# Performance work log

Hardware: AMD Instinct MI355X
Metric: run time of the kernel (lower is better)

The kernel has to match this reference:

```python
import jax, jax.numpy as jnp
import numpy as np

B, N, MODES, WIDTH = 4, 8192, 12, 32
TWO = 2 * MODES  # 24
M_TOT = TWO * (TWO - 1)  # 552


def setup_inputs() -> dict:
    key = jax.random.key(0)
    ks = jax.random.split(key, 12)
    scale = 1.0 / (WIDTH * WIDTH)
    x = jax.random.uniform(ks[0], (B, N, 2), jnp.float32)
    fc0_w = jax.random.normal(ks[1], (2, WIDTH), jnp.float32) * 0.1
    fc0_b = jax.random.normal(ks[2], (WIDTH,), jnp.float32) * 0.05
    # 4 layers x {weights1, weights2}, stored as real/imag pairs (torch.rand cfloat ~ U[0,1)+1j*U[0,1))
    spec_w = jax.random.uniform(ks[3], (4, 2, WIDTH, WIDTH, MODES, MODES, 2), jnp.float32) * scale
    conv_w = jax.random.normal(ks[4], (4, WIDTH, WIDTH), jnp.float32) * 0.1  # Conv1d k=1 -> [O,I]
    conv_b = jax.random.normal(ks[5], (4, WIDTH), jnp.float32) * 0.05
    fc1_w = jax.random.normal(ks[6], (WIDTH, 128), jnp.float32) * 0.1
    fc1_b = jax.random.normal(ks[7], (128,), jnp.float32) * 0.05
    fc2_w = jax.random.normal(ks[8], (128, 1), jnp.float32) * 0.1
    fc2_b = jax.random.normal(ks[9], (1,), jnp.float32) * 0.05
    return {"x": x, "fc0_w": fc0_w, "fc0_b": fc0_b, "spec_w": spec_w,
            "conv_w": conv_w, "conv_b": conv_b, "fc1_w": fc1_w, "fc1_b": fc1_b,
            "fc2_w": fc2_w, "fc2_b": fc2_b}


def _vft_matrices(xp, yp):
    # xp, yp: [B, N], already min-shifted and scaled to [0, 6.28]
    kx = jnp.concatenate([jnp.arange(MODES), jnp.arange(-MODES, 0)]).astype(jnp.float32)       # [24]
    ky = jnp.concatenate([jnp.arange(MODES), jnp.arange(-(MODES - 1), 0)]).astype(jnp.float32)  # [23]
    Xm = kx[None, :, None] * xp[:, None, :]  # [B,24,N]
    Ym = ky[None, :, None] * yp[:, None, :]  # [B,23,N]
    # torch: X repeat(1,23,1) tiles blocks; Y repeat(1,1,24).reshape interleaves -> row j*24+i = X[i]+Y[j]
    phase = jnp.tile(Xm, (1, TWO - 1, 1)) + jnp.repeat(Ym, TWO, axis=1)  # [B,552,N]
    V_fwd = jnp.exp(-1j * phase)                    # [B,552,N] complex64
    V_inv = jnp.conj(V_fwd).transpose(0, 2, 1)      # [B,N,552]
    return V_fwd, V_inv


def _spectral_conv(h, V_fwd, V_inv, w1, w2):
    # h: [B,C,N] real; w1,w2: [C,C,M,M] complex
    b, c, n = h.shape
    # forward Vandermonde transform: bmm(V_fwd, h^T) then permute -> [B,C,552]
    x_ft = jnp.einsum('bmn,bnc->bcm', V_fwd, h.astype(jnp.complex64).transpose(0, 2, 1))
    x_ft = x_ft.reshape(b, c, TWO, TWO - 1)
    top = jnp.einsum('bixy,ioxy->boxy', x_ft[:, :, :MODES, :MODES], w1)
    bot = jnp.einsum('bixy,ioxy->boxy', x_ft[:, :, -MODES:, :MODES], w2)
    out_ft = jnp.zeros((b, WIDTH, TWO, MODES), jnp.complex64)
    out_ft = out_ft.at[:, :, :MODES, :MODES].set(top)
    out_ft = out_ft.at[:, :, -MODES:, :MODES].set(bot)
    x_ft = out_ft.reshape(b, WIDTH, 2 * MODES * MODES)  # [B,C,288]
    # conjugate-symmetric completion (flip over last two dims, as in source)
    x_ft2 = jnp.conj(jnp.flip(x_ft[..., TWO:], axis=(-2, -1)))  # [B,C,264]
    x_ft = jnp.concatenate([x_ft, x_ft2], axis=-1)  # [B,C,552]
    out = jnp.einsum('bnm,bmc->bcn', V_inv, x_ft.transpose(0, 2, 1))  # [B,C,N]
    return (out / n * 2).real


def reference(x, fc0_w, fc0_b, spec_w, conv_w, conv_b, fc1_w, fc1_b, fc2_w, fc2_b):
    gelu = lambda t: jax.nn.gelu(t, approximate=False)
    # VFT mutates x in-place by subtracting global mins (view semantics in torch)
    xp = x[:, :, 0] - jnp.min(x[:, :, 0])
    yp = x[:, :, 1] - jnp.min(x[:, :, 1])
    x_in = jnp.stack([xp, yp], axis=-1)  # what fc0 actually sees
    V_fwd, V_inv = _vft_matrices(xp * 6.28 / jnp.max(xp), yp * 6.28 / jnp.max(yp))
    h = (x_in @ fc0_w + fc0_b).transpose(0, 2, 1)  # [B,C,N]
    for l in range(4):
        w1 = spec_w[l, 0, ..., 0] + 1j * spec_w[l, 0, ..., 1]
        w2 = spec_w[l, 1, ..., 0] + 1j * spec_w[l, 1, ..., 1]
        x1 = _spectral_conv(h, V_fwd, V_inv, w1, w2)
        x2 = jnp.einsum('bin,oi->bon', h, conv_w[l]) + conv_b[l][None, :, None]
        h = x1 + x2
        if l < 3:
            h = gelu(h)
    h = h.transpose(0, 2, 1)  # [B,N,C]
    h = gelu(h @ fc1_w + fc1_b)
    return h @ fc2_w + fc2_b  # [B,N,1]
```

## Files before the change

### kernel.cpp

```cpp
#include <hip/hip_runtime.h>
#include <cmath>

#define NB 4
#define NN 8192
#define CH 32

typedef short short8 __attribute__((ext_vector_type(8)));
typedef float floatx4 __attribute__((ext_vector_type(4)));
typedef unsigned short ushort_t;

__device__ __forceinline__ unsigned short f2b(float f){
  unsigned u = __float_as_uint(f);
  u = u + 0x7FFFu + ((u >> 16) & 1u);
  return (unsigned short)(u >> 16);
}
__device__ __forceinline__ float b2f(unsigned short h){
  return __uint_as_float(((unsigned)h) << 16);
}
__device__ __forceinline__ float gelu_f(float v){
  return 0.5f * v * (1.0f + erff(v * 0.70710678118654752440f));
}
__device__ __forceinline__ int repk(int t){
  int j = t / 24, i = t - j * 24;
  if(j == 0)  return (i <= 12) ? i : -1;
  if(j <= 11) return 13 + (j - 1) * 24 + i;
  return (i == 12) ? 277 + (j - 12) : -1;
}
__device__ __forceinline__ int partner(int t){
  int j = t / 24, i = t - j * 24;
  return ((23 - j) % 23) * 24 + ((24 - i) % 24);
}
__device__ __forceinline__ int repT(int k){
  if(k < 13) return k;
  if(k < 277){ int m = k - 13; return (m / 24 + 1) * 24 + (m % 24); }
  return (k - 277 + 12) * 24 + 12;
}

__global__ __launch_bounds__(256) void k_pre(const float* __restrict__ spec,
    float2* __restrict__ wt, const float* __restrict__ x, float4* __restrict__ pmm)
{
  const int tid = threadIdx.x;
  if(blockIdx.x < 128){
    int g = blockIdx.x * 256 + tid;
    float a = x[(size_t)g * 2], b = x[(size_t)g * 2 + 1];
    float mn0 = a, mx0 = a, mn1 = b, mx1 = b;
    for(int off = 32; off > 0; off >>= 1){
      mn0 = fminf(mn0, __shfl_down(mn0, off));
      mx0 = fmaxf(mx0, __shfl_down(mx0, off));
      mn1 = fminf(mn1, __shfl_down(mn1, off));
      mx1 = fmaxf(mx1, __shfl_down(mx1, off));
    }
    __shared__ float4 wp[4];
    if((tid & 63) == 0) wp[tid >> 6] = make_float4(mn0, mn1, mx0, mx1);
    __syncthreads();
    if(tid == 0){
      float4 r = wp[0];
      for(int i2 = 1; i2 < 4; ++i2){
        float4 v = wp[i2];
        r.x = fminf(r.x, v.x); r.y = fminf(r.y, v.y);
        r.z = fmaxf(r.z, v.z); r.w = fmaxf(r.w, v.w);
      }
      pmm[blockIdx.x] = r;
    }
  } else {
    int g = (blockIdx.x - 128) * 256 + tid;
    int o  = g & 31;
    int i  = (g >> 5) & 31;
    int rest = g >> 10;
    int pq = rest % 144;
    int ls = rest / 144;
    wt[g] = ((const float2*)spec)[(((size_t)(ls * 32 + i) * 32 + o) * 144 + pq)];
  }
}

__global__ __launch_bounds__(256) void k_vbuild(const float* __restrict__ x,
    const float4* __restrict__ pmm, const float* __restrict__ fw,
    const float* __restrict__ fb, ushort_t* __restrict__ AF, ushort_t* __restrict__ VTF,
    float* __restrict__ h, ushort_t* __restrict__ hb)
{
  __shared__ ushort_t lds1[32 * 584];
  __shared__ float4 mmv;
  const int tid = threadIdx.x;
  if(tid < 64){
    float4 a = pmm[tid], c = pmm[tid + 64];
    float mn0 = fminf(a.x, c.x), mn1 = fminf(a.y, c.y);
    float mx0 = fmaxf(a.z, c.z), mx1 = fmaxf(a.w, c.w);
    for(int off = 32; off > 0; off >>= 1){
      mn0 = fminf(mn0, __shfl_down(mn0, off));
      mn1 = fminf(mn1, __shfl_down(mn1, off));
      mx0 = fmaxf(mx0, __shfl_down(mx0, off));
      mx1 = fmaxf(mx1, __shfl_down(mx1, off));
    }
    if(tid == 0) mmv = make_float4(mn0, mn1, mx0, mx1);
  }
  __syncthreads();
  const int nl = tid & 31, part = tid >> 5;
  const int b = blockIdx.x >> 8;
  const int nblk = blockIdx.x & 255;
  const int n = nblk * 32 + nl;
  float mn0 = mmv.x, mn1 = mmv.y, mx0 = mmv.z, mx1 = mmv.w;
  float x0 = x[(size_t)(b * NN + n) * 2]     - mn0;
  float x1 = x[(size_t)(b * NN + n) * 2 + 1] - mn1;
  float sp = x0 * (6.28f / (mx0 - mn0));
  float sq = x1 * (6.28f / (mx1 - mn1));
  float cx, sx, cy, sy;
  sincosf(sp, &sx, &cx);
  sincosf(sq, &sy, &cy);
  int j0 = part * 3;
  int j1 = (j0 + 3 < 23) ? j0 + 3 : 23;
  float ky0 = (j0 < 12) ? (float)j0 : (float)(j0 - 23);
  float cb, sb;
  sincosf(ky0 * sq, &sb, &cb);
  for(int j = j0; j < j1; ++j){
    float ca = 1.0f, sa = 0.0f;
    #pragma unroll
    for(int i = 0; i < 24; ++i){
      float vr = ca * cb - sa * sb;
      float vi = -(sa * cb + ca * sb);
      int t = j * 24 + i;
      int k = repk(t);
      if(k >= 0){
        lds1[nl * 584 + k]       = f2b(vr);
        lds1[nl * 584 + 288 + k] = f2b(vi);
      }
      float cn = ca * cx - sa * sx;
      float sn = sa * cx + ca * sx;
      if(i == 11) sn = -sn;
      ca = cn; sa = sn;
    }
    float cbn = cb * cy - sb * sy;
    float sbn = sb * cy + cb * sy;
    cb = cbn; sb = sbn;
  }
  __syncthreads();
  #pragma unroll
  for(int r = 0; r < 9; ++r){
    int c = tid + 256 * r;
    int t16 = c / 1152;
    int c2 = c - t16 * 1152;
    int kk = c2 >> 6;
    int rem = c2 & 63;
    int q = rem >> 4, n15 = rem & 15;
    short8 v = *(const short8*)(lds1 + (t16 * 16 + n15) * 584 + kk * 32 + q * 8);
    *(short8*)(VTF + ((size_t)((b * 512 + nblk * 2 + t16) * 18 + kk)) * 512
               + (q * 16 + n15) * 8) = v;
  }
  #pragma unroll
  for(int r = 0; r < 9; ++r){
    int c = tid + 256 * r;
    int st = c >> 6;
    int rem = c & 63;
    int q = rem >> 4, srow = rem & 15;
    int sg = st * 16 + srow;
    int s = (sg < 288) ? sg : sg - 288;
    int sinh_ = (sg >= 288);
    int p2 = s / 12, qq = s - p2 * 12;
    int t = p2 * 23 + qq;
    int k = repk(t);
    unsigned short flip = 0;
    if(k < 0){ k = repk(partner(t)); if(sinh_) flip = 0x8000; }
    int col = sinh_ ? 288 + k : k;
    ushort_t tmp[8];
    #pragma unroll
    for(int e = 0; e < 8; ++e)
      tmp[e] = lds1[(q * 8 + e) * 584 + col] ^ flip;
    *(short8*)(AF + ((size_t)((b * 36 + st) * 256 + nblk)) * 512
               + (q * 16 + srow) * 8) = *(short8*)tmp;
  }
  #pragma unroll
  for(int rr = 0; rr < 4; ++rr){
    int c2 = (tid >> 5) + rr * 8;
    float v = fb[c2] + x0 * fw[c2] + x1 * fw[32 + c2];
    size_t idx = (size_t)(b * CH + c2) * NN + n;
    h[idx] = v; hb[idx] = f2b(v);
  }
}

__global__ __launch_bounds__(256) void k_fwd(const ushort_t* __restrict__ AF,
    const ushort_t* __restrict__ hb, float* __restrict__ xp)
{
  const int stp = blockIdx.x;
  const int ks = blockIdx.y;
  const int b  = blockIdx.z;
  const int w = threadIdx.x >> 6;
  const int lane = threadIdx.x & 63;
  const int row = lane & 15;
  const int q = lane >> 4;
  const int st0 = stp * 2;
  const size_t abase0 = ((size_t)(b * 36 + st0) * 256) * 512 + (q * 16 + row) * 8;
  const size_t abase1 = abase0 + (size_t)256 * 512;
  const size_t hb0 = (size_t)(b * CH + row) * NN;
  const size_t hb1 = hb0 + (size_t)16 * NN;
  floatx4 aA0 = {0.f,0.f,0.f,0.f}, aA1 = {0.f,0.f,0.f,0.f};
  floatx4 aB0 = {0.f,0.f,0.f,0.f}, aB1 = {0.f,0.f,0.f,0.f};
  #pragma unroll
  for(int kk = 0; kk < 8; ++kk){
    int g = ks * 32 + w * 8 + kk;
    short8 A0 = *(const short8*)(AF + abase0 + (size_t)g * 512);
    short8 A1 = *(const short8*)(AF + abase1 + (size_t)g * 512);
    int nn2 = g * 32 + q * 8;
    short8 B0 = *(const short8*)(hb + hb0 + nn2);
    short8 B1 = *(const short8*)(hb + hb1 + nn2);
    aA0 = __builtin_amdgcn_mfma_f32_16x16x32_bf16(A0, B0, aA0, 0, 0, 0);
    aA1 = __builtin_amdgcn_mfma_f32_16x16x32_bf16(A0, B1, aA1, 0, 0, 0);
    aB0 = __builtin_amdgcn_mfma_f32_16x16x32_bf16(A1, B0, aB0, 0, 0, 0);
    aB1 = __builtin_amdgcn_mfma_f32_16x16x32_bf16(A1, B1, aB1, 0, 0, 0);
  }
  __shared__ float red[4 * 512];
  const int e = threadIdx.x;
  #pragma unroll
  for(int r = 0; r < 4; ++r){
    int rrow = q * 4 + r;
    red[w * 512 + rrow * 32 + row]      = aA0[r];
    red[w * 512 + rrow * 32 + 16 + row] = aA1[r];
  }
  __syncthreads();
  {
    float v0 = red[e] + red[512 + e] + red[1024 + e] + red[1536 + e];
    float v1 = red[e + 256] + red[512 + e + 256] + red[1024 + e + 256] + red[1536 + e + 256];
    size_t base = ((size_t)(ks * NB + b) * 576 + st0 * 16) * 32;
    xp[base + e] = v0;
    xp[base + e + 256] = v1;
  }
  __syncthreads();
  #pragma unroll
  for(int r = 0; r < 4; ++r){
    int rrow = q * 4 + r;
    red[w * 512 + rrow * 32 + row]      = aB0[r];
    red[w * 512 + rrow * 32 + 16 + row] = aB1[r];
  }
  __syncthreads();
  {
    float v0 = red[e] + red[512 + e] + red[1024 + e] + red[1536 + e];
    float v1 = red[e + 256] + red[512 + e + 256] + red[1024 + e + 256] + red[1536 + e + 256];
    size_t base = ((size_t)(ks * NB + b) * 576 + (st0 + 1) * 16) * 32;
    xp[base + e] = v0;
    xp[base + e + 256] = v1;
  }
}

__global__ __launch_bounds__(256) void k_mixg(const float* __restrict__ xp,
    const float2* __restrict__ wt, ushort_t* __restrict__ ghi, ushort_t* __restrict__ glo,
    int layer)
{
  const int w = threadIdx.x >> 6;
  const int lane = threadIdx.x & 63;
  const int k = blockIdx.x * 4 + w;
  const int b = blockIdx.y;
  const int t = repT(k);
  const int j = t / 24, i = t - j * 24;
  const int u = partner(t);
  const bool unpaired = (i == 12) || (u == t);
  const int idxT = (t < 288) ? t : 575 - t;  const bool cfT = (t >= 288);
  const int idxU = (u < 288) ? u : 575 - u;  const bool cfU = (u >= 288);
  __shared__ float Xs[4][2][64];
  const int o = lane & 31, half = lane >> 5;
  #pragma unroll
  for(int m = 0; m < 2; ++m){
    int idx = m ? idxU : idxT;
    int rrow = half ? 288 + idx : idx;
    float s = 0.f;
    #pragma unroll
    for(int ks = 0; ks < 8; ++ks)
      s += xp[((size_t)(ks * NB + b) * 576 + rrow) * 32 + o];
    Xs[w][m][half * 32 + o] = s;
  }
  __syncthreads();
  float Fr[2], Fi[2];
  #pragma unroll
  for(int m = 0; m < 2; ++m){
    int idx = m ? idxU : idxT;
    int p2 = idx / 12, qq = idx - p2 * 12;
    int sel = (p2 < 12) ? 0 : 1;
    int pq = (p2 % 12) * 12 + qq;
    const float2* wb = wt + ((size_t)((layer * 2 + sel) * 144 + pq)) * 1024;
    int i0 = half * 16;
    float fr = 0.f, fi = 0.f;
    #pragma unroll
    for(int ii = 0; ii < 16; ++ii){
      int i2 = i0 + ii;
      float xr = Xs[w][m][i2], xi = Xs[w][m][32 + i2];
      float2 wv = wb[i2 * 32 + o];
      fr += xr * wv.x - xi * wv.y;
      fi += xr * wv.y + xi * wv.x;
    }
    fr += __shfl_down(fr, 32);
    fi += __shfl_down(fi, 32);
    Fr[m] = fr; Fi[m] = fi;
  }
  const int c = lane & 31;
  const int srcT = cfT ? 31 - c : c;
  const int srcU = cfU ? 31 - c : c;
  float fax = __shfl(Fr[0], srcT);
  float fay = __shfl(Fi[0], srcT);
  float fbx = __shfl(Fr[1], srcU);
  float fby = __shfl(Fi[1], srcU);
  if(lane < 32){
    float gr = fax;
    float gi = cfT ? -fay : fay;
    if(!unpaired){
      gr += fbx;
      gi -= (cfU ? -fby : fby);
    }
    unsigned short hr = f2b(gr); float lr = gr - b2f(hr);
    unsigned short hi2 = f2b(gi); float li = gi - b2f(hi2);
    size_t base = (size_t)(b * CH + c) * 576;
    ghi[base + k] = hr;          ghi[base + 288 + k] = hi2;
    glo[base + k] = f2b(lr);     glo[base + 288 + k] = f2b(li);
  }
}

template<int LAST>
__global__ __launch_bounds__(512, 2) void k_inv(const ushort_t* __restrict__ VTF,
    const ushort_t* __restrict__ ghi, const ushort_t* __restrict__ glo,
    const float* __restrict__ hfull, const float* __restrict__ cw,
    const float* __restrict__ cbias, float* __restrict__ hout,
    ushort_t* __restrict__ houtb, int layer,
    const float* __restrict__ w1, const float* __restrict__ b1,
    const float* __restrict__ w2, const float* __restrict__ b2,
    float* __restrict__ out)
{
  __shared__ ushort_t GH[32][584];
  __shared__ ushort_t GL[32][584];
  __shared__ float hTc[32][129];
  __shared__ float Wl[1024];
  __shared__ float Bl[32];
  const int tid = threadIdx.x;
  const int b = blockIdx.y;
  const int n0 = blockIdx.x * 128;
  for(int idx = tid; idx < 2304; idx += 512){
    int ch = idx / 72, g8 = (idx - ch * 72) * 8;
    size_t src = (size_t)(b * CH + ch) * 576 + g8;
    *(short8*)&GH[ch][g8] = *(const short8*)(ghi + src);
    *(short8*)&GL[ch][g8] = *(const short8*)(glo + src);
  }
  {
    int ch = tid >> 4, grp = tid & 15;
    const float* src = hfull + (size_t)(b * CH + ch) * NN + n0 + grp * 8;
    float4 v0 = *(const float4*)src;
    float4 v1 = *(const float4*)(src + 4);
    int p = grp * 8;
    hTc[ch][p + 0] = v0.x; hTc[ch][p + 1] = v0.y;
    hTc[ch][p + 2] = v0.z; hTc[ch][p + 3] = v0.w;
    hTc[ch][p + 4] = v1.x; hTc[ch][p + 5] = v1.y;
    hTc[ch][p + 6] = v1.z; hTc[ch][p + 7] = v1.w;
  }
  for(int idx = tid; idx < 1024; idx += 512)
    Wl[(idx & 31) * 32 + (idx >> 5)] = cw[layer * 1024 + idx];
  if(tid < 32) Bl[tid] = cbias[layer * 32 + tid];
  __syncthreads();
  const int lane = tid & 63;
  const int w = tid >> 6;
  const int row = lane & 15;
  const int q = lane >> 4;
  const int nloc = w * 16 + row;
  const int n = n0 + nloc;
  const int n16 = blockIdx.x * 8 + w;
  const ushort_t* vb = VTF + ((size_t)(b * 512 + n16) * 18) * 512 + (q * 16 + row) * 8;
  const int ko = q * 8;
  floatx4 acc0 = {0.f,0.f,0.f,0.f}, acc1 = {0.f,0.f,0.f,0.f};
  #pragma unroll
  for(int kk = 0; kk < 18; ++kk){
    short8 Bv  = *(const short8*)(vb + (size_t)kk * 512);
    short8 Ah0 = *(const short8*)&GH[row][ko + kk * 32];
    short8 Al0 = *(const short8*)&GL[row][ko + kk * 32];
    short8 Ah1 = *(const short8*)&GH[16 + row][ko + kk * 32];
    short8 Al1 = *(const short8*)&GL[16 + row][ko + kk * 32];
    acc0 = __builtin_amdgcn_mfma_f32_16x16x32_bf16(Ah0, Bv, acc0, 0, 0, 0);
    acc0 = __builtin_amdgcn_mfma_f32_16x16x32_bf16(Al0, Bv, acc0, 0, 0, 0);
    acc1 = __builtin_amdgcn_mfma_f32_16x16x32_bf16(Ah1, Bv, acc1, 0, 0, 0);
    acc1 = __builtin_amdgcn_mfma_f32_16x16x32_bf16(Al1, Bv, acc1, 0, 0, 0);
  }
  float acc2[8];
  {
    const int c0 = q * 4;
    #pragma unroll
    for(int r = 0; r < 4; ++r){ acc2[r] = Bl[c0 + r]; acc2[4 + r] = Bl[16 + c0 + r]; }
    #pragma unroll
    for(int i = 0; i < CH; ++i){
      float hv = hTc[i][nloc];
      float4 wv0 = *(const float4*)&Wl[i * 32 + c0];
      float4 wv1 = *(const float4*)&Wl[i * 32 + 16 + c0];
      acc2[0] = fmaf(hv, wv0.x, acc2[0]);
      acc2[1] = fmaf(hv, wv0.y, acc2[1]);
      acc2[2] = fmaf(hv, wv0.z, acc2[2]);
      acc2[3] = fmaf(hv, wv0.w, acc2[3]);
      acc2[4] = fmaf(hv, wv1.x, acc2[4]);
      acc2[5] = fmaf(hv, wv1.y, acc2[5]);
      acc2[6] = fmaf(hv, wv1.z, acc2[6]);
      acc2[7] = fmaf(hv, wv1.w, acc2[7]);
    }
  }
  const float sc = 2.0f / 8192.0f;
  if constexpr(!LAST){
    #pragma unroll
    for(int r = 0; r < 4; ++r){
      int c = q * 4 + r;
      float v0 = gelu_f(acc0[r] * sc + acc2[r]);
      size_t idx0 = (size_t)(b * CH + c) * NN + n;
      hout[idx0] = v0; houtb[idx0] = f2b(v0);
      float v1 = gelu_f(acc1[r] * sc + acc2[4 + r]);
      size_t idx1 = (size_t)(b * CH + 16 + c) * NN + n;
      hout[idx1] = v1; houtb[idx1] = f2b(v1);
    }
  } else {
    __shared__ float hT2[128][33];
    __shared__ float Wfc1[4096];
    __shared__ float b1s[128], w2s[128];
    __shared__ float red2[512];
    #pragma unroll
    for(int r = 0; r < 4; ++r){
      int c = q * 4 + r;
      hT2[nloc][c]      = acc0[r] * sc + acc2[r];
      hT2[nloc][16 + c] = acc1[r] * sc + acc2[4 + r];
    }
    for(int idx2 = tid; idx2 < 4096; idx2 += 512) Wfc1[idx2] = w1[idx2];
    if(tid < 128){ b1s[tid] = b1[tid]; w2s[tid] = w2[tid]; }
    __syncthreads();
    const int nl2 = tid & 127;
    const int js = tid >> 7;
    float acc3 = 0.f;
    for(int jj = js * 32; jj < js * 32 + 32; ++jj){
      float s = b1s[jj];
      #pragma unroll
      for(int i = 0; i < CH; ++i) s = fmaf(hT2[nl2][i], Wfc1[i * 128 + jj], s);
      acc3 = fmaf(gelu_f(s), w2s[jj], acc3);
    }
    red2[tid] = acc3;
    __syncthreads();
    if(js == 0){
      float v = red2[nl2] + red2[nl2 + 128] + red2[nl2 + 256] + red2[nl2 + 384] + b2[0];
      out[(size_t)b * NN + n0 + nl2] = v;
    }
  }
}

extern "C" void kernel_launch(void* const* d_in, const int* in_sizes, int n_in,
                              void* d_out, int out_size, void* d_ws, size_t ws_size,
                              hipStream_t stream)
{
  const float* x      = (const float*)d_in[0];
  const float* fc0_w  = (const float*)d_in[1];
  const float* fc0_b  = (const float*)d_in[2];
  const float* spec_w = (const float*)d_in[3];
  const float* conv_w = (const float*)d_in[4];
  const float* conv_b = (const float*)d_in[5];
  const float* fc1_w  = (const float*)d_in[6];
  const float* fc1_b  = (const float*)d_in[7];
  const float* fc2_w  = (const float*)d_in[8];
  const float* fc2_b  = (const float*)d_in[9];
  float* out = (float*)d_out;

  char* w = (char*)d_ws;
  const size_t OFF_PMM  = 0;
  const size_t OFF_WT   = 4096;
  const size_t OFF_AF   = OFF_WT  + 9437184;
  const size_t OFF_VTF  = OFF_AF  + 37748736;
  const size_t OFF_H0   = OFF_VTF + 37748736;
  const size_t OFF_H1   = OFF_H0  + 4194304;
  const size_t OFF_H0B  = OFF_H1  + 4194304;
  const size_t OFF_H1B  = OFF_H0B + 2097152;
  const size_t OFF_XP   = OFF_H1B + 2097152;
  const size_t OFF_GHI  = OFF_XP  + 2359296;
  const size_t OFF_GLO  = OFF_GHI + 147456;

  float4* pmm    = (float4*)(w + OFF_PMM);
  float2* wt     = (float2*)(w + OFF_WT);
  ushort_t* AF   = (ushort_t*)(w + OFF_AF);
  ushort_t* VTF  = (ushort_t*)(w + OFF_VTF);
  float* hbuf[2]     = { (float*)(w + OFF_H0), (float*)(w + OFF_H1) };
  ushort_t* hbufb[2] = { (ushort_t*)(w + OFF_H0B), (ushort_t*)(w + OFF_H1B) };
  float* xp      = (float*)(w + OFF_XP);
  ushort_t* ghi  = (ushort_t*)(w + OFF_GHI);
  ushort_t* glo  = (ushort_t*)(w + OFF_GLO);

  hipLaunchKernelGGL(k_pre, dim3(4736), dim3(256), 0, stream, spec_w, wt, x, pmm);
  hipLaunchKernelGGL(k_vbuild, dim3(1024), dim3(256), 0, stream, x, pmm,
                     fc0_w, fc0_b, AF, VTF, hbuf[0], hbufb[0]);

  for(int l = 0; l < 4; ++l){
    int in = l & 1, outb = 1 - in;
    hipLaunchKernelGGL(k_fwd, dim3(18, 8, NB), dim3(256), 0, stream, AF, hbufb[in], xp);
    hipLaunchKernelGGL(k_mixg, dim3(72, NB), dim3(256), 0, stream, xp, wt, ghi, glo, l);
    if(l < 3)
      hipLaunchKernelGGL(k_inv<0>, dim3(64, NB), dim3(512), 0, stream, VTF, ghi, glo,
                         hbuf[in], conv_w, conv_b, hbuf[outb], hbufb[outb], l,
                         fc1_w, fc1_b, fc2_w, fc2_b, out);
    else
      hipLaunchKernelGGL(k_inv<1>, dim3(64, NB), dim3(512), 0, stream, VTF, ghi, glo,
                         hbuf[in], conv_w, conv_b, hbuf[outb], hbufb[outb], l,
                         fc1_w, fc1_b, fc2_w, fc2_b, out);
  }
  (void)in_sizes; (void)n_in; (void)out_size; (void)ws_size;
}
```

Before: 256.2 us.

## Fuse all stages into one cooperative persistent kernel with grid syncs

```diff
diff --git a/kernel.cpp b/kernel.cpp
--- a/kernel.cpp
+++ b/kernel.cpp
@@ -1,5 +1,8 @@
 #include <hip/hip_runtime.h>
+#include <hip/hip_cooperative_groups.h>
 #include <cmath>
+
+namespace cg = cooperative_groups;
 
 #define NB 4
 #define NN 8192
@@ -36,34 +39,49 @@
   return (k - 277 + 12) * 24 + 12;
 }
 
-__global__ __launch_bounds__(256) void k_pre(const float* __restrict__ spec,
-    float2* __restrict__ wt, const float* __restrict__ x, float4* __restrict__ pmm)
+#define SMEM_BYTES 95488
+
+__global__ __launch_bounds__(512, 2) void k_mega(
+    const float* __restrict__ x, const float* __restrict__ fc0w,
+    const float* __restrict__ fc0b, const float* __restrict__ spec,
+    const float* __restrict__ convw, const float* __restrict__ convb,
+    const float* __restrict__ w1, const float* __restrict__ b1,
+    const float* __restrict__ w2, const float* __restrict__ b2,
+    float* __restrict__ out,
+    float2* __restrict__ wt, float4* __restrict__ pmm,
+    ushort_t* __restrict__ AF, ushort_t* __restrict__ VTF,
+    float* __restrict__ h0, float* __restrict__ h1,
+    ushort_t* __restrict__ h0b, ushort_t* __restrict__ h1b,
+    float* __restrict__ xp, ushort_t* __restrict__ ghi, ushort_t* __restrict__ glo)
 {
+  __shared__ __align__(16) char smem[SMEM_BYTES];
+  cg::grid_group grid = cg::this_grid();
   const int tid = threadIdx.x;
-  if(blockIdx.x < 128){
-    int g = blockIdx.x * 256 + tid;
-    float a = x[(size_t)g * 2], b = x[(size_t)g * 2 + 1];
-    float mn0 = a, mx0 = a, mn1 = b, mx1 = b;
+
+  if(blockIdx.x < 64){
+    int g = blockIdx.x * 512 + tid;
+    float a = x[(size_t)g * 2], bb = x[(size_t)g * 2 + 1];
+    float mn0 = a, mx0 = a, mn1 = bb, mx1 = bb;
     for(int off = 32; off > 0; off >>= 1){
       mn0 = fminf(mn0, __shfl_down(mn0, off));
       mx0 = fmaxf(mx0, __shfl_down(mx0, off));
       mn1 = fminf(mn1, __shfl_down(mn1, off));
       mx1 = fmaxf(mx1, __shfl_down(mx1, off));
     }
-    __shared__ float4 wp[4];
+    float4* wp = (float4*)smem;
     if((tid & 63) == 0) wp[tid >> 6] = make_float4(mn0, mn1, mx0, mx1);
     __syncthreads();
     if(tid == 0){
       float4 r = wp[0];
-      for(int i2 = 1; i2 < 4; ++i2){
+      for(int i2 = 1; i2 < 8; ++i2){
         float4 v = wp[i2];
         r.x = fminf(r.x, v.x); r.y = fminf(r.y, v.y);
         r.z = fmaxf(r.z, v.z); r.w = fmaxf(r.w, v.w);
       }
       pmm[blockIdx.x] = r;
     }
-  } else {
-    int g = (blockIdx.x - 128) * 256 + tid;
+  }
+  for(int g = blockIdx.x * 512 + tid; g < 1179648; g += 131072){
     int o  = g & 31;
     int i  = (g >> 5) & 31;
     int rest = g >> 10;
@@ -71,367 +89,380 @@
     int ls = rest / 144;
     wt[g] = ((const float2*)spec)[(((size_t)(ls * 32 + i) * 32 + o) * 144 + pq)];
   }
-}
-
-__global__ __launch_bounds__(256) void k_vbuild(const float* __restrict__ x,
-    const float4* __restrict__ pmm, const float* __restrict__ fw,
-    const float* __restrict__ fb, ushort_t* __restrict__ AF, ushort_t* __restrict__ VTF,
-    float* __restrict__ h, ushort_t* __restrict__ hb)
-{
-  __shared__ ushort_t lds1[32 * 584];
-  __shared__ float4 mmv;
-  const int tid = threadIdx.x;
-  if(tid < 64){
-    float4 a = pmm[tid], c = pmm[tid + 64];
-    float mn0 = fminf(a.x, c.x), mn1 = fminf(a.y, c.y);
-    float mx0 = fmaxf(a.z, c.z), mx1 = fmaxf(a.w, c.w);
-    for(int off = 32; off > 0; off >>= 1){
-      mn0 = fminf(mn0, __shfl_down(mn0, off));
-      mn1 = fminf(mn1, __shfl_down(mn1, off));
-      mx0 = fmaxf(mx0, __shfl_down(mx0, off));
-      mx1 = fmaxf(mx1, __shfl_down(mx1, off));
-    }
-    if(tid == 0) mmv = make_float4(mn0, mn1, mx0, mx1);
+  grid.sync();
+
+  {
+    float4* mmvp = (float4*)(smem + 74752);
+    if(tid < 64){
+      float4 a = pmm[tid];
+      float mn0 = a.x, mn1 = a.y, mx0 = a.z, mx1 = a.w;
+      for(int off = 32; off > 0; off >>= 1){
+        mn0 = fminf(mn0, __shfl_down(mn0, off));
+        mn1 = fminf(mn1, __shfl_down(mn1, off));
+        mx0 = fmaxf(mx0, __shfl_down(mx0, off));
+        mx1 = fmaxf(mx1, __shfl_down(mx1, off));
+      }
+      if(tid == 0) *mmvp = make_float4(mn0, mn1, mx0, mx1);
+    }
+    __syncthreads();
+    const float4 mm = *mmvp;
+    ushort_t* lds1 = (ushort_t*)smem;
+    const int nl = tid & 63, part = tid >> 6;
+    for(int it = 0; it < 2; ++it){
+      int sblk = blockIdx.x * 2 + it;
+      int b = sblk >> 7;
+      int sb = sblk & 127;
+      int n0 = sb * 64;
+      int n = n0 + nl;
+      float x0 = x[(size_t)(b * NN + n) * 2]     - mm.x;
+      float x1 = x[(size_t)(b * NN + n) * 2 + 1] - mm.y;
+      float sp = x0 * (6.28f / (mm.z - mm.x));
+      float sq = x1 * (6.28f / (mm.w - mm.y));
+      float cx, sx, cy, sy;
+      sincosf(sp, &sx, &cx);
+      sincosf(sq, &sy, &cy);
+      int j0 = part * 3;
+      int j1 = (j0 + 3 < 23) ? j0 + 3 : 23;
+      float ky0 = (j0 < 12) ? (float)j0 : (float)(j0 - 23);
+      float cb, sb2;
+      sincosf(ky0 * sq, &sb2, &cb);
+      for(int j = j0; j < j1; ++j){
+        float ca = 1.0f, sa = 0.0f;
+        #pragma unroll
+        for(int i = 0; i < 24; ++i){
+          float vr = ca * cb - sa * sb2;
+          float vi = -(sa * cb + ca * sb2);
+          int t = j * 24 + i;
+          int k = repk(t);
+          if(k >= 0){
+            lds1[nl * 584 + k]       = f2b(vr);
+            lds1[nl * 584 + 288 + k] = f2b(vi);
+          }
+          float cn = ca * cx - sa * sx;
+          float sn = sa * cx + ca * sx;
+          if(i == 11) sn = -sn;
+          ca = cn; sa = sn;
+        }
+        float cbn = cb * cy - sb2 * sy;
+        float sbn = sb2 * cy + cb * sy;
+        cb = cbn; sb2 = sbn;
+      }
+      __syncthreads();
+      #pragma unroll
+      for(int r = 0; r < 9; ++r){
+        int c = tid + 512 * r;
+        int t16 = c / 1152;
+        int c2 = c - t16 * 1152;
+        int kk = c2 >> 6;
+        int rem = c2 & 63;
+        int q = rem >> 4, n15 = rem & 15;
+        short8 v = *(const short8*)(lds1 + (t16 * 16 + n15) * 584 + kk * 32 + q * 8);
+        *(short8*)(VTF + ((size_t)((b * 512 + sb * 4 + t16) * 18 + kk)) * 512
+                   + (q * 16 + n15) * 8) = v;
+      }
+      #pragma unroll
+      for(int r = 0; r < 9; ++r){
+        int c = tid + 512 * r;
+        int hh = c / 2304;
+        int c2 = c - hh * 2304;
+        int st = c2 >> 6;
+        int rem = c2 & 63;
+        int q = rem >> 4, srow = rem & 15;
+        int sg = st * 16 + srow;
+        int s = (sg < 288) ? sg : sg - 288;
+        int sinh_ = (sg >= 288);
+        int p2 = s / 12, qq = s - p2 * 12;
+        int t = p2 * 23 + qq;
+        int k = repk(t);
+        unsigned short flip = 0;
+        if(k < 0){ k = repk(partner(t)); if(sinh_) flip = 0x8000; }
+        int col = sinh_ ? 288 + k : k;
+        ushort_t tmp[8];
+        #pragma unroll
+        for(int e = 0; e < 8; ++e)
+          tmp[e] = lds1[(hh * 32 + q * 8 + e) * 584 + col] ^ flip;
+        *(short8*)(AF + ((size_t)((b * 36 + st) * 256 + sb * 2 + hh)) * 512
+                   + (q * 16 + srow) * 8) = *(short8*)tmp;
+      }
+      #pragma unroll
+      for(int rr = 0; rr < 4; ++rr){
+        int c2 = part + rr * 8;
+        float v = fc0b[c2] + x0 * fc0w[c2] + x1 * fc0w[32 + c2];
+        size_t idx = (size_t)(b * CH + c2) * NN + n;
+        h0[idx] = v; h0b[idx] = f2b(v);
+      }
+      __syncthreads();
+    }
   }
-  __syncthreads();
-  const int nl = tid & 31, part = tid >> 5;
-  const int b = blockIdx.x >> 8;
-  const int nblk = blockIdx.x & 255;
-  const int n = nblk * 32 + nl;
-  float mn0 = mmv.x, mn1 = mmv.y, mx0 = mmv.z, mx1 = mmv.w;
-  float x0 = x[(size_t)(b * NN + n) * 2]     - mn0;
-  float x1 = x[(size_t)(b * NN + n) * 2 + 1] - mn1;
-  float sp = x0 * (6.28f / (mx0 - mn0));
-  float sq = x1 * (6.28f / (mx1 - mn1));
-  float cx, sx, cy, sy;
-  sincosf(sp, &sx, &cx);
-  sincosf(sq, &sy, &cy);
-  int j0 = part * 3;
-  int j1 = (j0 + 3 < 23) ? j0 + 3 : 23;
-  float ky0 = (j0 < 12) ? (float)j0 : (float)(j0 - 23);
-  float cb, sb;
-  sincosf(ky0 * sq, &sb, &cb);
-  for(int j = j0; j < j1; ++j){
-    float ca = 1.0f, sa = 0.0f;
-    #pragma unroll
-    for(int i = 0; i < 24; ++i){
-      float vr = ca * cb - sa * sb;
-      float vi = -(sa * cb + ca * sb);
-      int t = j * 24 + i;
-      int k = repk(t);
-      if(k >= 0){
-        lds1[nl * 584 + k]       = f2b(vr);
-        lds1[nl * 584 + 288 + k] = f2b(vi);
-      }
-      float cn = ca * cx - sa * sx;
-      float sn = sa * cx + ca * sx;
-      if(i == 11) sn = -sn;
-      ca = cn; sa = sn;
-    }
-    float cbn = cb * cy - sb * sy;
-    float sbn = sb * cy + cb * sy;
-    cb = cbn; sb = sbn;
-  }
-  __syncthreads();
-  #pragma unroll
-  for(int r = 0; r < 9; ++r){
-    int c = tid + 256 * r;
-    int t16 = c / 1152;
-    int c2 = c - t16 * 1152;
-    int kk = c2 >> 6;
-    int rem = c2 & 63;
-    int q = rem >> 4, n15 = rem & 15;
-    short8 v = *(const short8*)(lds1 + (t16 * 16 + n15) * 584 + kk * 32 + q * 8);
-    *(short8*)(VTF + ((size_t)((b * 512 + nblk * 2 + t16) * 18 + kk)) * 512
-               + (q * 16 + n15) * 8) = v;
-  }
-  #pragma unroll
-  for(int r = 0; r < 9; ++r){
-    int c = tid + 256 * r;
-    int st = c >> 6;
-    int rem = c & 63;
-    int q = rem >> 4, srow = rem & 15;
-    int sg = st * 16 + srow;
-    int s = (sg < 288) ? sg : sg - 288;
-    int sinh_ = (sg >= 288);
-    int p2 = s / 12, qq = s - p2 * 12;
-    int t = p2 * 23 + qq;
-    int k = repk(t);
-    unsigned short flip = 0;
-    if(k < 0){ k = repk(partner(t)); if(sinh_) flip = 0x8000; }
-    int col = sinh_ ? 288 + k : k;
-    ushort_t tmp[8];
-    #pragma unroll
-    for(int e = 0; e < 8; ++e)
-      tmp[e] = lds1[(q * 8 + e) * 584 + col] ^ flip;
-    *(short8*)(AF + ((size_t)((b * 36 + st) * 256 + nblk)) * 512
-               + (q * 16 + srow) * 8) = *(short8*)tmp;
-  }
-  #pragma unroll
-  for(int rr = 0; rr < 4; ++rr){
-    int c2 = (tid >> 5) + rr * 8;
-    float v = fb[c2] + x0 * fw[c2] + x1 * fw[32 + c2];
-    size_t idx = (size_t)(b * CH + c2) * NN + n;
-    h[idx] = v; hb[idx] = f2b(v);
-  }
-}
-
-__global__ __launch_bounds__(256) void k_fwd(const ushort_t* __restrict__ AF,
-    const ushort_t* __restrict__ hb, float* __restrict__ xp)
-{
-  const int stp = blockIdx.x;
-  const int ks = blockIdx.y;
-  const int b  = blockIdx.z;
-  const int w = threadIdx.x >> 6;
-  const int lane = threadIdx.x & 63;
-  const int row = lane & 15;
-  const int q = lane >> 4;
-  const int st0 = stp * 2;
-  const size_t abase0 = ((size_t)(b * 36 + st0) * 256) * 512 + (q * 16 + row) * 8;
-  const size_t abase1 = abase0 + (size_t)256 * 512;
-  const size_t hb0 = (size_t)(b * CH + row) * NN;
-  const size_t hb1 = hb0 + (size_t)16 * NN;
-  floatx4 aA0 = {0.f,0.f,0.f,0.f}, aA1 = {0.f,0.f,0.f,0.f};
-  floatx4 aB0 = {0.f,0.f,0.f,0.f}, aB1 = {0.f,0.f,0.f,0.f};
-  #pragma unroll
-  for(int kk = 0; kk < 8; ++kk){
-    int g = ks * 32 + w * 8 + kk;
-    short8 A0 = *(const short8*)(AF + abase0 + (size_t)g * 512);
-    short8 A1 = *(const short8*)(AF + abase1 + (size_t)g * 512);
-    int nn2 = g * 32 + q * 8;
-    short8 B0 = *(const short8*)(hb + hb0 + nn2);
-    short8 B1 = *(const short8*)(hb + hb1 + nn2);
-    aA0 = __builtin_amdgcn_mfma_f32_16x16x32_bf16(A0, B0, aA0, 0, 0, 0);
-    aA1 = __builtin_amdgcn_mfma_f32_16x16x32_bf16(A0, B1, aA1, 0, 0, 0);
-    aB0 = __builtin_amdgcn_mfma_f32_16x16x32_bf16(A1, B0, aB0, 0, 0, 0);
-    aB1 = __builtin_amdgcn_mfma_f32_16x16x32_bf16(A1, B1, aB1, 0, 0, 0);
-  }
-  __shared__ float red[4 * 512];
-  const int e = threadIdx.x;
-  #pragma unroll
-  for(int r = 0; r < 4; ++r){
-    int rrow = q * 4 + r;
-    red[w * 512 + rrow * 32 + row]      = aA0[r];
-    red[w * 512 + rrow * 32 + 16 + row] = aA1[r];
-  }
-  __syncthreads();
-  {
-    float v0 = red[e] + red[512 + e] + red[1024 + e] + red[1536 + e];
-    float v1 = red[e + 256] + red[512 + e + 256] + red[1024 + e + 256] + red[1536 + e + 256];
-    size_t base = ((size_t)(ks * NB + b) * 576 + st0 * 16) * 32;
-    xp[base + e] = v0;
-    xp[base + e + 256] = v1;
-  }
-  __syncthreads();
-  #pragma unroll
-  for(int r = 0; r < 4; ++r){
-    int rrow = q * 4 + r;
-    red[w * 512 + rrow * 32 + row]      = aB0[r];
-    red[w * 512 + rrow * 32 + 16 + row] = aB1[r];
-  }
-  __syncthreads();
-  {
-    float v0 = red[e] + red[512 + e] + red[1024 + e] + red[1536 + e];
-    float v1 = red[e + 256] + red[512 + e + 256] + red[1024 + e + 256] + red[1536 + e + 256];
-    size_t base = ((size_t)(ks * NB + b) * 576 + (st0 + 1) * 16) * 32;
-    xp[base + e] = v0;
-    xp[base + e + 256] = v1;
-  }
-}
-
-__global__ __launch_bounds__(256) void k_mixg(const float* __restrict__ xp,
-    const float2* __restrict__ wt, ushort_t* __restrict__ ghi, ushort_t* __restrict__ glo,
-    int layer)
-{
-  const int w = threadIdx.x >> 6;
-  const int lane = threadIdx.x & 63;
-  const int k = blockIdx.x * 4 + w;
-  const int b = blockIdx.y;
-  const int t = repT(k);
-  const int j = t / 24, i = t - j * 24;
-  const int u = partner(t);
-  const bool unpaired = (i == 12) || (u == t);
-  const int idxT = (t < 288) ? t : 575 - t;  const bool cfT = (t >= 288);
-  const int idxU = (u < 288) ? u : 575 - u;  const bool cfU = (u >= 288);
-  __shared__ float Xs[4][2][64];
-  const int o = lane & 31, half = lane >> 5;
-  #pragma unroll
-  for(int m = 0; m < 2; ++m){
-    int idx = m ? idxU : idxT;
-    int rrow = half ? 288 + idx : idx;
-    float s = 0.f;
-    #pragma unroll
-    for(int ks = 0; ks < 8; ++ks)
-      s += xp[((size_t)(ks * NB + b) * 576 + rrow) * 32 + o];
-    Xs[w][m][half * 32 + o] = s;
-  }
-  __syncthreads();
-  float Fr[2], Fi[2];
-  #pragma unroll
-  for(int m = 0; m < 2; ++m){
-    int idx = m ? idxU : idxT;
-    int p2 = idx / 12, qq = idx - p2 * 12;
-    int sel = (p2 < 12) ? 0 : 1;
-    int pq = (p2 % 12) * 12 + qq;
-    const float2* wb = wt + ((size_t)((layer * 2 + sel) * 144 + pq)) * 1024;
-    int i0 = half * 16;
-    float fr = 0.f, fi = 0.f;
-    #pragma unroll
-    for(int ii = 0; ii < 16; ++ii){
-      int i2 = i0 + ii;
-      float xr = Xs[w][m][i2], xi = Xs[w][m][32 + i2];
-      float2 wv = wb[i2 * 32 + o];
-      fr += xr * wv.x - xi * wv.y;
-      fi += xr * wv.y + xi * wv.x;
-    }
-    fr += __shfl_down(fr, 32);
-    fi += __shfl_down(fi, 32);
-    Fr[m] = fr; Fi[m] = fi;
-  }
-  const int c = lane & 31;
-  const int srcT = cfT ? 31 - c : c;
-  const int srcU = cfU ? 31 - c : c;
-  float fax = __shfl(Fr[0], srcT);
-  float fay = __shfl(Fi[0], srcT);
-  float fbx = __shfl(Fr[1], srcU);
-  float fby = __shfl(Fi[1], srcU);
-  if(lane < 32){
-    float gr = fax;
-    float gi = cfT ? -fay : fay;
-    if(!unpaired){
-      gr += fbx;
-      gi -= (cfU ? -fby : fby);
-    }
-    unsigned short hr = f2b(gr); float lr = gr - b2f(hr);
-    unsigned short hi2 = f2b(gi); float li = gi - b2f(hi2);
-    size_t base = (size_t)(b * CH + c) * 576;
-    ghi[base + k] = hr;          ghi[base + 288 + k] = hi2;
-    glo[base + k] = f2b(lr);     glo[base + 288 + k] = f2b(li);
-  }
-}
-
-template<int LAST>
-__global__ __launch_bounds__(512, 2) void k_inv(const ushort_t* __restrict__ VTF,
-    const ushort_t* __restrict__ ghi, const ushort_t* __restrict__ glo,
-    const float* __restrict__ hfull, const float* __restrict__ cw,
-    const float* __restrict__ cbias, float* __restrict__ hout,
-    ushort_t* __restrict__ houtb, int layer,
-    const float* __restrict__ w1, const float* __restrict__ b1,
-    const float* __restrict__ w2, const float* __restrict__ b2,
-    float* __restrict__ out)
-{
-  __shared__ ushort_t GH[32][584];
-  __shared__ ushort_t GL[32][584];
-  __shared__ float hTc[32][129];
-  __shared__ float Wl[1024];
-  __shared__ float Bl[32];
-  const int tid = threadIdx.x;
-  const int b = blockIdx.y;
-  const int n0 = blockIdx.x * 128;
-  for(int idx = tid; idx < 2304; idx += 512){
-    int ch = idx / 72, g8 = (idx - ch * 72) * 8;
-    size_t src = (size_t)(b * CH + ch) * 576 + g8;
-    *(short8*)&GH[ch][g8] = *(const short8*)(ghi + src);
-    *(short8*)&GL[ch][g8] = *(const short8*)(glo + src);
-  }
-  {
-    int ch = tid >> 4, grp = tid & 15;
-    const float* src = hfull + (size_t)(b * CH + ch) * NN + n0 + grp * 8;
-    float4 v0 = *(const float4*)src;
-    float4 v1 = *(const float4*)(src + 4);
-    int p = grp * 8;
-    hTc[ch][p + 0] = v0.x; hTc[ch][p + 1] = v0.y;
-    hTc[ch][p + 2] = v0.z; hTc[ch][p + 3] = v0.w;
-    hTc[ch][p + 4] = v1.x; hTc[ch][p + 5] = v1.y;
-    hTc[ch][p + 6] = v1.z; hTc[ch][p + 7] = v1.w;
-  }
-  for(int idx = tid; idx < 1024; idx += 512)
-    Wl[(idx & 31) * 32 + (idx >> 5)] = cw[layer * 1024 + idx];
-  if(tid < 32) Bl[tid] = cbias[layer * 32 + tid];
-  __syncthreads();
-  const int lane = tid & 63;
-  const int w = tid >> 6;
-  const int row = lane & 15;
-  const int q = lane >> 4;
-  const int nloc = w * 16 + row;
-  const int n = n0 + nloc;
-  const int n16 = blockIdx.x * 8 + w;
-  const ushort_t* vb = VTF + ((size_t)(b * 512 + n16) * 18) * 512 + (q * 16 + row) * 8;
-  const int ko = q * 8;
-  floatx4 acc0 = {0.f,0.f,0.f,0.f}, acc1 = {0.f,0.f,0.f,0.f};
-  #pragma unroll
-  for(int kk = 0; kk < 18; ++kk){
-    short8 Bv  = *(const short8*)(vb + (size_t)kk * 512);
-    short8 Ah0 = *(const short8*)&GH[row][ko + kk * 32];
-    short8 Al0 = *(const short8*)&GL[row][ko + kk * 32];
-    short8 Ah1 = *(const short8*)&GH[16 + row][ko + kk * 32];
-    short8 Al1 = *(const short8*)&GL[16 + row][ko + kk * 32];
-    acc0 = __builtin_amdgcn_mfma_f32_16x16x32_bf16(Ah0, Bv, acc0, 0, 0, 0);
-    acc0 = __builtin_amdgcn_mfma_f32_16x16x32_bf16(Al0, Bv, acc0, 0, 0, 0);
-    acc1 = __builtin_amdgcn_mfma_f32_16x16x32_bf16(Ah1, Bv, acc1, 0, 0, 0);
-    acc1 = __builtin_amdgcn_mfma_f32_16x16x32_bf16(Al1, Bv, acc1, 0, 0, 0);
-  }
-  float acc2[8];
-  {
-    const int c0 = q * 4;
-    #pragma unroll
-    for(int r = 0; r < 4; ++r){ acc2[r] = Bl[c0 + r]; acc2[4 + r] = Bl[16 + c0 + r]; }
-    #pragma unroll
-    for(int i = 0; i < CH; ++i){
-      float hv = hTc[i][nloc];
-      float4 wv0 = *(const float4*)&Wl[i * 32 + c0];
-      float4 wv1 = *(const float4*)&Wl[i * 32 + 16 + c0];
-      acc2[0] = fmaf(hv, wv0.x, acc2[0]);
-      acc2[1] = fmaf(hv, wv0.y, acc2[1]);
-      acc2[2] = fmaf(hv, wv0.z, acc2[2]);
-      acc2[3] = fmaf(hv, wv0.w, acc2[3]);
-      acc2[4] = fmaf(hv, wv1.x, acc2[4]);
-      acc2[5] = fmaf(hv, wv1.y, acc2[5]);
-      acc2[6] = fmaf(hv, wv1.z, acc2[6]);
-      acc2[7] = fmaf(hv, wv1.w, acc2[7]);
-    }
-  }
-  const float sc = 2.0f / 8192.0f;
-  if constexpr(!LAST){
-    #pragma unroll
-    for(int r = 0; r < 4; ++r){
-      int c = q * 4 + r;
-      float v0 = gelu_f(acc0[r] * sc + acc2[r]);
-      size_t idx0 = (size_t)(b * CH + c) * NN + n;
-      hout[idx0] = v0; houtb[idx0] = f2b(v0);
-      float v1 = gelu_f(acc1[r] * sc + acc2[4 + r]);
-      size_t idx1 = (size_t)(b * CH + 16 + c) * NN + n;
-      hout[idx1] = v1; houtb[idx1] = f2b(v1);
-    }
-  } else {
-    __shared__ float hT2[128][33];
-    __shared__ float Wfc1[4096];
-    __shared__ float b1s[128], w2s[128];
-    __shared__ float red2[512];
-    #pragma unroll
-    for(int r = 0; r < 4; ++r){
-      int c = q * 4 + r;
-      hT2[nloc][c]      = acc0[r] * sc + acc2[r];
-      hT2[nloc][16 + c] = acc1[r] * sc + acc2[4 + r];
-    }
-    for(int idx2 = tid; idx2 < 4096; idx2 += 512) Wfc1[idx2] = w1[idx2];
-    if(tid < 128){ b1s[tid] = b1[tid]; w2s[tid] = w2[tid]; }
-    __syncthreads();
-    const int nl2 = tid & 127;
-    const int js = tid >> 7;
-    float acc3 = 0.f;
-    for(int jj = js * 32; jj < js * 32 + 32; ++jj){
-      float s = b1s[jj];
+  grid.sync();
+
+  for(int l = 0; l < 4; ++l){
+    const float* hin      = (l & 1) ? h1  : h0;
+    const ushort_t* hbin  = (l & 1) ? h1b : h0b;
+    float* hout           = (l & 1) ? h0  : h1;
+    ushort_t* houtb       = (l & 1) ? h0b : h1b;
+    const int last = (l == 3);
+
+    {
+      const int grp = tid >> 8;
+      const int tg = tid & 255;
+      const int w4 = tg >> 6;
+      const int lane = tg & 63;
+      const int row = lane & 15;
+      const int q = lane >> 4;
+      float* red = (float*)smem + grp * 2048;
+      for(int t = blockIdx.x * 2 + grp; t < 576; t += 512){
+        __syncthreads();
+        int stp = t % 18;
+        int ks = (t / 18) & 7;
+        int b = t / 144;
+        const int st0 = stp * 2;
+        const size_t abase0 = ((size_t)(b * 36 + st0) * 256) * 512 + (q * 16 + row) * 8;
+        const size_t abase1 = abase0 + (size_t)256 * 512;
+        const size_t hb0 = (size_t)(b * CH + row) * NN;
+        const size_t hb1 = hb0 + (size_t)16 * NN;
+        floatx4 aA0 = {0.f,0.f,0.f,0.f}, aA1 = {0.f,0.f,0.f,0.f};
+        floatx4 aB0 = {0.f,0.f,0.f,0.f}, aB1 = {0.f,0.f,0.f,0.f};
+        #pragma unroll
+        for(int kk = 0; kk < 8; ++kk){
+          int g = ks * 32 + w4 * 8 + kk;
+          short8 A0 = *(const short8*)(AF + abase0 + (size_t)g * 512);
+          short8 A1 = *(const short8*)(AF + abase1 + (size_t)g * 512);
+          int nn2 = g * 32 + q * 8;
+          short8 B0 = *(const short8*)(hbin + hb0 + nn2);
+          short8 B1 = *(const short8*)(hbin + hb1 + nn2);
+          aA0 = __builtin_amdgcn_mfma_f32_16x16x32_bf16(A0, B0, aA0, 0, 0, 0);
+          aA1 = __builtin_amdgcn_mfma_f32_16x16x32_bf16(A0, B1, aA1, 0, 0, 0);
+          aB0 = __builtin_amdgcn_mfma_f32_16x16x32_bf16(A1, B0, aB0, 0, 0, 0);
+          aB1 = __builtin_amdgcn_mfma_f32_16x16x32_bf16(A1, B1, aB1, 0, 0, 0);
+        }
+        const int e = tg;
+        #pragma unroll
+        for(int r = 0; r < 4; ++r){
+          int rrow = q * 4 + r;
+          red[w4 * 512 + rrow * 32 + row]      = aA0[r];
+          red[w4 * 512 + rrow * 32 + 16 + row] = aA1[r];
+        }
+        __syncthreads();
+        {
+          float v0 = red[e] + red[512 + e] + red[1024 + e] + red[1536 + e];
+          float v1 = red[e + 256] + red[512 + e + 256] + red[1024 + e + 256] + red[1536 + e + 256];
+          size_t base = ((size_t)(ks * NB + b) * 576 + st0 * 16) * 32;
+          xp[base + e] = v0;
+          xp[base + e + 256] = v1;
+        }
+        __syncthreads();
+        #pragma unroll
+        for(int r = 0; r < 4; ++r){
+          int rrow = q * 4 + r;
+          red[w4 * 512 + rrow * 32 + row]      = aB0[r];
+          red[w4 * 512 + rrow * 32 + 16 + row] = aB1[r];
+        }
+        __syncthreads();
+        {
+          float v0 = red[e] + red[512 + e] + red[1024 + e] + red[1536 + e];
+          float v1 = red[e + 256] + red[512 + e + 256] + red[1024 + e + 256] + red[1536 + e + 256];
+          size_t base = ((size_t)(ks * NB + b) * 576 + (st0 + 1) * 16) * 32;
+          xp[base + e] = v0;
+          xp[base + e + 256] = v1;
+        }
+      }
+    }
+    grid.sync();
+
+    {
+      const int w = tid >> 6;
+      const int lane = tid & 63;
+      const int gw = blockIdx.x * 8 + w;
+      const bool act = gw < 1152;
+      const int k = act ? gw % 288 : 0;
+      const int b = act ? gw / 288 : 0;
+      const int t = repT(k);
+      const int jj2 = t / 24, ii2 = t - jj2 * 24;
+      const int u = partner(t);
+      const bool unpaired = (ii2 == 12) || (u == t);
+      const int idxT = (t < 288) ? t : 575 - t;  const bool cfT = (t >= 288);
+      const int idxU = (u < 288) ? u : 575 - u;  const bool cfU = (u >= 288);
+      float* XsW = (float*)smem + w * 128;
+      const int o = lane & 31, half = lane >> 5;
+      if(act){
+        #pragma unroll
+        for(int m = 0; m < 2; ++m){
+          int idx = m ? idxU : idxT;
+          int rrow = half ? 288 + idx : idx;
+          float s = 0.f;
+          #pragma unroll
+          for(int ks = 0; ks < 8; ++ks)
+            s += xp[((size_t)(ks * NB + b) * 576 + rrow) * 32 + o];
+          XsW[m * 64 + half * 32 + o] = s;
+        }
+      }
+      __syncthreads();
+      if(act){
+        float Fr[2], Fi[2];
+        #pragma unroll
+        for(int m = 0; m < 2; ++m){
+          int idx = m ? idxU : idxT;
+          int p2 = idx / 12, qq = idx - p2 * 12;
+          int sel = (p2 < 12) ? 0 : 1;
+          int pq = (p2 % 12) * 12 + qq;
+          const float2* wb = wt + ((size_t)((l * 2 + sel) * 144 + pq)) * 1024;
+          int i0 = half * 16;
+          float fr = 0.f, fi = 0.f;
+          #pragma unroll
+          for(int ii = 0; ii < 16; ++ii){
+            int i2 = i0 + ii;
+            float xr = XsW[m * 64 + i2], xi = XsW[m * 64 + 32 + i2];
+            float2 wv = wb[i2 * 32 + o];
+            fr += xr * wv.x - xi * wv.y;
+            fi += xr * wv.y + xi * wv.x;
+          }
+          fr += __shfl_down(fr, 32);
+          fi += __shfl_down(fi, 32);
+          Fr[m] = fr; Fi[m] = fi;
+        }
+        const int c = lane & 31;
+        const int srcT = cfT ? 31 - c : c;
+        const int srcU = cfU ? 31 - c : c;
+        float fax = __shfl(Fr[0], srcT);
+        float fay = __shfl(Fi[0], srcT);
+        float fbx = __shfl(Fr[1], srcU);
+        float fby = __shfl(Fi[1], srcU);
+        if(lane < 32){
+          float gr = fax;
+          float gi = cfT ? -fay : fay;
+          if(!unpaired){
+            gr += fbx;
+            gi -= (cfU ? -fby : fby);
+          }
+          unsigned short hr = f2b(gr); float lr = gr - b2f(hr);
+          unsigned short hi2 = f2b(gi); float li = gi - b2f(hi2);
+          size_t base = (size_t)(b * CH + c) * 576;
+          ghi[base + k] = hr;          ghi[base + 288 + k] = hi2;
+          glo[base + k] = f2b(lr);     glo[base + 288 + k] = f2b(li);
+        }
+      }
+    }
+    grid.sync();
+
+    {
+      ushort_t (*GH)[584] = (ushort_t(*)[584])smem;
+      ushort_t (*GL)[584] = (ushort_t(*)[584])(smem + 37376);
+      float (*hTc)[129]   = (float(*)[129])(smem + 74752);
+      float* Wl           = (float*)(smem + 91264);
+      float* Bl           = (float*)(smem + 95360);
+      const int bx = blockIdx.x & 63;
+      const int b = blockIdx.x >> 6;
+      const int n0 = bx * 128;
+      for(int idx = tid; idx < 2304; idx += 512){
+        int ch = idx / 72, g8 = (idx - ch * 72) * 8;
+        size_t src = (size_t)(b * CH + ch) * 576 + g8;
+        *(short8*)&GH[ch][g8] = *(const short8*)(ghi + src);
+        *(short8*)&GL[ch][g8] = *(const short8*)(glo + src);
+      }
+      {
+        int ch = tid >> 4, grp = tid & 15;
+        const float* src = hin + (size_t)(b * CH + ch) * NN + n0 + grp * 8;
+        float4 v0 = *(const float4*)src;
+        float4 v1 = *(const float4*)(src + 4);
+        int p = grp * 8;
+        hTc[ch][p + 0] = v0.x; hTc[ch][p + 1] = v0.y;
+        hTc[ch][p + 2] = v0.z; hTc[ch][p + 3] = v0.w;
+        hTc[ch][p + 4] = v1.x; hTc[ch][p + 5] = v1.y;
+        hTc[ch][p + 6] = v1.z; hTc[ch][p + 7] = v1.w;
+      }
+      for(int idx = tid; idx < 1024; idx += 512)
+        Wl[(idx & 31) * 32 + (idx >> 5)] = convw[l * 1024 + idx];
+      if(tid < 32) Bl[tid] = convb[l * 32 + tid];
+      __syncthreads();
+      const int lane = tid & 63;
+      const int wv = tid >> 6;
+      const int row = lane & 15;
+      const int q = lane >> 4;
+      const int nloc = wv * 16 + row;
+      const int n = n0 + nloc;
+      const int n16 = bx * 8 + wv;
+      const ushort_t* vb = VTF + ((size_t)(b * 512 + n16) * 18) * 512 + (q * 16 + row) * 8;
+      const int ko = q * 8;
+      floatx4 acc0 = {0.f,0.f,0.f,0.f}, acc1 = {0.f,0.f,0.f,0.f};
       #pragma unroll
-      for(int i = 0; i < CH; ++i) s = fmaf(hT2[nl2][i], Wfc1[i * 128 + jj], s);
-      acc3 = fmaf(gelu_f(s), w2s[jj], acc3);
-    }
-    red2[tid] = acc3;
-    __syncthreads();
-    if(js == 0){
-      float v = red2[nl2] + red2[nl2 + 128] + red2[nl2 + 256] + red2[nl2 + 384] + b2[0];
-      out[(size_t)b * NN + n0 + nl2] = v;
-    }
+      for(int kk = 0; kk < 18; ++kk){
+        short8 Bv  = *(const short8*)(vb + (size_t)kk * 512);
+        short8 Ah0 = *(const short8*)&GH[row][ko + kk * 32];
+        short8 Al0 = *(const short8*)&GL[row][ko + kk * 32];
+        short8 Ah1 = *(const short8*)&GH[16 + row][ko + kk * 32];
+        short8 Al1 = *(const short8*)&GL[16 + row][ko + kk * 32];
+        acc0 = __builtin_amdgcn_mfma_f32_16x16x32_bf16(Ah0, Bv, acc0, 0, 0, 0);
+        acc0 = __builtin_amdgcn_mfma_f32_16x16x32_bf16(Al0, Bv, acc0, 0, 0, 0);
+        acc1 = __builtin_amdgcn_mfma_f32_16x16x32_bf16(Ah1, Bv, acc1, 0, 0, 0);
+        acc1 = __builtin_amdgcn_mfma_f32_16x16x32_bf16(Al1, Bv, acc1, 0, 0, 0);
+      }
+      float acc2[8];
+      {
+        const int c0 = q * 4;
+        #pragma unroll
+        for(int r = 0; r < 4; ++r){ acc2[r] = Bl[c0 + r]; acc2[4 + r] = Bl[16 + c0 + r]; }
+        #pragma unroll
+        for(int i = 0; i < CH; ++i){
+          float hv = hTc[i][nloc];
+          float4 wv0 = *(const float4*)&Wl[i * 32 + c0];
+          float4 wv1 = *(const float4*)&Wl[i * 32 + 16 + c0];
+          acc2[0] = fmaf(hv, wv0.x, acc2[0]);
+          acc2[1] = fmaf(hv, wv0.y, acc2[1]);
+          acc2[2] = fmaf(hv, wv0.z, acc2[2]);
+          acc2[3] = fmaf(hv, wv0.w, acc2[3]);
+          acc2[4] = fmaf(hv, wv1.x, acc2[4]);
+          acc2[5] = fmaf(hv, wv1.y, acc2[5]);
+          acc2[6] = fmaf(hv, wv1.z, acc2[6]);
+          acc2[7] = fmaf(hv, wv1.w, acc2[7]);
+        }
+      }
+      const float sc = 2.0f / 8192.0f;
+      if(!last){
+        #pragma unroll
+        for(int r = 0; r < 4; ++r){
+          int c = q * 4 + r;
+          float v0 = gelu_f(acc0[r] * sc + acc2[r]);
+          size_t idx0 = (size_t)(b * CH + c) * NN + n;
+          hout[idx0] = v0; houtb[idx0] = f2b(v0);
+          float v1 = gelu_f(acc1[r] * sc + acc2[4 + r]);
+          size_t idx1 = (size_t)(b * CH + 16 + c) * NN + n;
+          hout[idx1] = v1; houtb[idx1] = f2b(v1);
+        }
+      } else {
+        __syncthreads();
+        float (*hT2)[33] = (float(*)[33])smem;
+        float* Wfc1 = (float*)(smem + 16896);
+        float* b1s  = (float*)(smem + 33280);
+        float* w2s  = (float*)(smem + 33792);
+        float* red2 = (float*)(smem + 34304);
+        #pragma unroll
+        for(int r = 0; r < 4; ++r){
+          int c = q * 4 + r;
+          hT2[nloc][c]      = acc0[r] * sc + acc2[r];
+          hT2[nloc][16 + c] = acc1[r] * sc + acc2[4 + r];
+        }
+        for(int idx2 = tid; idx2 < 4096; idx2 += 512) Wfc1[idx2] = w1[idx2];
+        if(tid < 128){ b1s[tid] = b1[tid]; w2s[tid] = w2[tid]; }
+        __syncthreads();
+        const int nl2 = tid & 127;
+        const int js = tid >> 7;
+        float acc3 = 0.f;
+        for(int jj = js * 32; jj < js * 32 + 32; ++jj){
+          float s = b1s[jj];
+          #pragma unroll
+          for(int i = 0; i < CH; ++i) s = fmaf(hT2[nl2][i], Wfc1[i * 128 + jj], s);
+          acc3 = fmaf(gelu_f(s), w2s[jj], acc3);
+        }
+        red2[tid] = acc3;
+        __syncthreads();
+        if(js == 0){
+          float v = red2[nl2] + red2[nl2 + 128] + red2[nl2 + 256] + red2[nl2 + 384] + b2[0];
+          out[(size_t)b * NN + n0 + nl2] = v;
+        }
+      }
+    }
+    if(l < 3) grid.sync();
   }
 }
 
@@ -468,28 +499,23 @@
   float2* wt     = (float2*)(w + OFF_WT);
   ushort_t* AF   = (ushort_t*)(w + OFF_AF);
   ushort_t* VTF  = (ushort_t*)(w + OFF_VTF);
-  float* hbuf[2]     = { (float*)(w + OFF_H0), (float*)(w + OFF_H1) };
-  ushort_t* hbufb[2] = { (ushort_t*)(w + OFF_H0B), (ushort_t*)(w + OFF_H1B) };
+  float* h0      = (float*)(w + OFF_H0);
+  float* h1      = (float*)(w + OFF_H1);
+  ushort_t* h0b  = (ushort_t*)(w + OFF_H0B);
+  ushort_t* h1b  = (ushort_t*)(w + OFF_H1B);
   float* xp      = (float*)(w + OFF_XP);
   ushort_t* ghi  = (ushort_t*)(w + OFF_GHI);
   ushort_t* glo  = (ushort_t*)(w + OFF_GLO);
 
-  hipLaunchKernelGGL(k_pre, dim3(4736), dim3(256), 0, stream, spec_w, wt, x, pmm);
-  hipLaunchKernelGGL(k_vbuild, dim3(1024), dim3(256), 0, stream, x, pmm,
-                     fc0_w, fc0_b, AF, VTF, hbuf[0], hbufb[0]);
-
-  for(int l = 0; l < 4; ++l){
-    int in = l & 1, outb = 1 - in;
-    hipLaunchKernelGGL(k_fwd, dim3(18, 8, NB), dim3(256), 0, stream, AF, hbufb[in], xp);
-    hipLaunchKernelGGL(k_mixg, dim3(72, NB), dim3(256), 0, stream, xp, wt, ghi, glo, l);
-    if(l < 3)
-      hipLaunchKernelGGL(k_inv<0>, dim3(64, NB), dim3(512), 0, stream, VTF, ghi, glo,
-                         hbuf[in], conv_w, conv_b, hbuf[outb], hbufb[outb], l,
-                         fc1_w, fc1_b, fc2_w, fc2_b, out);
-    else
-      hipLaunchKernelGGL(k_inv<1>, dim3(64, NB), dim3(512), 0, stream, VTF, ghi, glo,
-                         hbuf[in], conv_w, conv_b, hbuf[outb], hbufb[outb], l,
-                         fc1_w, fc1_b, fc2_w, fc2_b, out);
-  }
+  void* args[] = {
+    (void*)&x, (void*)&fc0_w, (void*)&fc0_b, (void*)&spec_w,
+    (void*)&conv_w, (void*)&conv_b, (void*)&fc1_w, (void*)&fc1_b,
+    (void*)&fc2_w, (void*)&fc2_b, (void*)&out,
+    (void*)&wt, (void*)&pmm, (void*)&AF, (void*)&VTF,
+    (void*)&h0, (void*)&h1, (void*)&h0b, (void*)&h1b,
+    (void*)&xp, (void*)&ghi, (void*)&glo
+  };
+  hipLaunchCooperativeKernel((const void*)k_mega, dim3(256), dim3(512),
+                             args, 0, stream);
   (void)in_sizes; (void)n_in; (void)out_size; (void)ws_size;
 }
```

New measurement: 662.4 us. 159% more time.
